# Performance work log

Measured on AMD Instinct MI355X. Metric: run time of the kernel, lower is better.

## Reference

```python
import jax, jax.numpy as jnp
import numpy as np

IMG_SIZE = 640


def _decode_level(cls, box, img_size):
    """cls: [B,C,H,W] logits, box: [B,4,H,W] offsets -> ([B,HW,4], [B,HW,1], [B,HW])."""
    B = cls.shape[0]
    cls = jnp.transpose(cls, (0, 2, 3, 1))          # [B,H,W,C]
    box = jnp.transpose(box, (0, 2, 3, 1))          # [B,H,W,4]
    prob = jax.nn.sigmoid(cls)
    conf = jnp.max(prob, axis=-1, keepdims=True)    # [B,H,W,1]
    cidx = jnp.argmax(prob, axis=-1)                # [B,H,W]
    stage = box.shape[1]                            # H (== W)
    step = img_size // stage                        # stride for this level
    grid = jnp.arange(stage, dtype=box.dtype) * step
    gx, gy = jnp.meshgrid(grid, grid, indexing='xy')
    block = jnp.stack([gx, gy], axis=-1)            # [H,W,2] anchor-point coords
    tl = block - box[..., :2]                       # x1,y1
    br = block + box[..., 2:4]                      # x2,y2
    boxes = jnp.concatenate([tl, br], axis=-1).reshape(B, -1, 4)
    scores = conf.reshape(B, -1, 1)
    classes = cidx.reshape(B, -1).astype(jnp.int64)
    return boxes, scores, classes


def setup_inputs() -> dict:
    key = jax.random.key(0)
    ks = jax.random.split(key, 6)
    return {
        'cls0': jax.random.normal(ks[0], (64, 80, 80, 80), dtype=jnp.float32),
        'box0': jax.random.uniform(ks[1], (64, 4, 80, 80), dtype=jnp.float32) * 32.0,
        'cls1': jax.random.normal(ks[2], (64, 80, 40, 40), dtype=jnp.float32),
        'box1': jax.random.uniform(ks[3], (64, 4, 40, 40), dtype=jnp.float32) * 64.0,
        'cls2': jax.random.normal(ks[4], (64, 80, 20, 20), dtype=jnp.float32),
        'box2': jax.random.uniform(ks[5], (64, 4, 20, 20), dtype=jnp.float32) * 128.0,
    }


def reference(cls0, box0, cls1, box1, cls2, box2):
    levels = [(cls0, box0), (cls1, box1), (cls2, box2)]
    boxes_l, scores_l, classes_l = [], [], []
    for cls, box in levels:
        b, s, c = _decode_level(cls, box, IMG_SIZE)
        boxes_l.append(b)
        scores_l.append(s)
        classes_l.append(c)
    boxes = jnp.concatenate(boxes_l, axis=1)      # [B,N,4]
    scores = jnp.concatenate(scores_l, axis=1)    # [B,N,1]
    classes = jnp.concatenate(classes_l, axis=1)  # [B,N]
    boxes = jnp.clip(boxes, 0.0, IMG_SIZE - 1)
    return boxes, scores, classes
```

## Files before the change

kernel.cpp:

```cpp
#include <hip/hip_runtime.h>
#include <cmath>


constexpr int B_   = 64;
constexpr int NC   = 80;
constexpr int NTOT = 8400;

__device__ __forceinline__ float sigmoidf_(float x) { return 1.0f / (1.0f + __expf(-x)); }

template<int HW, int W, int STEP, int NOFF>
__device__ __forceinline__ void decode_level(
    const float* __restrict__ cls, const float* __restrict__ box,
    float* __restrict__ oboxes, float* __restrict__ oscores, float* __restrict__ oclasses,
    int lbid, int tid)
{
    constexpr int PPI = HW / 2;

    int t = lbid * 256 + tid;
    int b = t / PPI;
    int p = (t - b * PPI) << 1;
    int h = p / W;
    int w = p - h * W;

    const float* bbase = box + (size_t)b * 4 * HW + p;
    float2 bl = *reinterpret_cast<const float2*>(bbase);
    float2 bt = *reinterpret_cast<const float2*>(bbase + HW);
    float2 br = *reinterpret_cast<const float2*>(bbase + 2 * HW);
    float2 bd = *reinterpret_cast<const float2*>(bbase + 3 * HW);

    const float* cbase = cls + (size_t)b * NC * HW + p;
    float m[2]  = {-3.4e38f, -3.4e38f};
    int   ci[2] = {0, 0};
    #pragma unroll 16
    for (int c = 0; c < NC; ++c) {
        float2 v = *reinterpret_cast<const float2*>(cbase + (size_t)c * HW);
        if (v.x > m[0]) { m[0] = v.x; ci[0] = c; }
        if (v.y > m[1]) { m[1] = v.y; ci[1] = c; }
    }

    size_t obase = (size_t)b * NTOT + NOFF + p;
    *reinterpret_cast<float2*>(oscores  + obase) = make_float2(sigmoidf_(m[0]), sigmoidf_(m[1]));
    *reinterpret_cast<float2*>(oclasses + obase) = make_float2((float)ci[0], (float)ci[1]);

    float gy = (float)(h * STEP);
    #pragma unroll
    for (int j = 0; j < 2; ++j) {
        float gx = (float)((w + j) * STEP);
        float l  = j ? bl.y : bl.x;
        float tt = j ? bt.y : bt.x;
        float r  = j ? br.y : br.x;
        float dd = j ? bd.y : bd.x;
        float4 o;
        o.x = fminf(fmaxf(gx - l,  0.0f), 639.0f);
        o.y = fminf(fmaxf(gy - tt, 0.0f), 639.0f);
        o.z = fminf(fmaxf(gx + r,  0.0f), 639.0f);
        o.w = fminf(fmaxf(gy + dd, 0.0f), 639.0f);
        *reinterpret_cast<float4*>(oboxes + (obase + j) * 4) = o;
    }
}

__global__ __launch_bounds__(256) void rtmdet_decode_fused(
    const float* __restrict__ cls0, const float* __restrict__ box0,
    const float* __restrict__ cls1, const float* __restrict__ box1,
    const float* __restrict__ cls2, const float* __restrict__ box2,
    float* __restrict__ oboxes, float* __restrict__ oscores, float* __restrict__ oclasses)
{
    int bid = blockIdx.x;
    int tid = threadIdx.x;
    if (bid < 800) {
        decode_level<6400, 80,  8,    0>(cls0, box0, oboxes, oscores, oclasses, bid,        tid);
    } else if (bid < 1000) {
        decode_level<1600, 40, 16, 6400>(cls1, box1, oboxes, oscores, oclasses, bid - 800,  tid);
    } else {
        decode_level< 400, 20, 32, 8000>(cls2, box2, oboxes, oscores, oclasses, bid - 1000, tid);
    }
}

extern "C" void kernel_launch(void* const* d_in, const int* in_sizes, int n_in,
                              void* d_out, int out_size, void* d_ws, size_t ws_size,
                              hipStream_t stream) {
    const float* cls0 = (const float*)d_in[0];
    const float* box0 = (const float*)d_in[1];
    const float* cls1 = (const float*)d_in[2];
    const float* box1 = (const float*)d_in[3];
    const float* cls2 = (const float*)d_in[4];
    const float* box2 = (const float*)d_in[5];

    float* oboxes   = (float*)d_out;
    float* oscores  = oboxes  + (size_t)B_ * NTOT * 4;
    float* oclasses = oscores + (size_t)B_ * NTOT;

    rtmdet_decode_fused<<<1050, 256, 0, stream>>>(cls0, box0, cls1, box1, cls2, box2,
                                                  oboxes, oscores, oclasses);
}
```

Measured before the change: 33.67 us.

## Split class reduction across two half-blocks with float4 loads and LDS merge

Each block now covers 512 positions as 128 quads. The two halves of the block each take 40 of the 80 classes and read them with float4 loads, then merge their max and argmax through shared memory after a barrier. Box decoding keeps its original pairwise mapping. The intent is wider 16-byte loads and a shorter serial per-thread loop, in exchange for a __syncthreads, LDS traffic, and half the threads sitting idle during the final score write. Grid size and total traffic are unchanged.

```diff
diff --git a/kernel.cpp b/kernel.cpp
--- a/kernel.cpp
+++ b/kernel.cpp
@@ -12,50 +12,86 @@
 __device__ __forceinline__ void decode_level(
     const float* __restrict__ cls, const float* __restrict__ box,
     float* __restrict__ oboxes, float* __restrict__ oscores, float* __restrict__ oclasses,
-    int lbid, int tid)
+    int lbid, int tid,
+    float (* __restrict__ sm)[256], int* __restrict__ spk)
 {
+    constexpr int QPI = HW / 4;
     constexpr int PPI = HW / 2;
 
-    int t = lbid * 256 + tid;
-    int b = t / PPI;
-    int p = (t - b * PPI) << 1;
-    int h = p / W;
-    int w = p - h * W;
+    int half = tid >> 7;
+    int lp   = tid & 127;
+    int quad = lbid * 128 + lp;
+    int b    = quad / QPI;
+    int p    = (quad - b * QPI) << 2;
 
-    const float* bbase = box + (size_t)b * 4 * HW + p;
-    float2 bl = *reinterpret_cast<const float2*>(bbase);
-    float2 bt = *reinterpret_cast<const float2*>(bbase + HW);
-    float2 br = *reinterpret_cast<const float2*>(bbase + 2 * HW);
-    float2 bd = *reinterpret_cast<const float2*>(bbase + 3 * HW);
-
-    const float* cbase = cls + (size_t)b * NC * HW + p;
-    float m[2]  = {-3.4e38f, -3.4e38f};
-    int   ci[2] = {0, 0};
-    #pragma unroll 16
-    for (int c = 0; c < NC; ++c) {
-        float2 v = *reinterpret_cast<const float2*>(cbase + (size_t)c * HW);
-        if (v.x > m[0]) { m[0] = v.x; ci[0] = c; }
-        if (v.y > m[1]) { m[1] = v.y; ci[1] = c; }
+    const float* cbase = cls + (size_t)b * NC * HW + (size_t)(half * 40) * HW + p;
+    float m[4]  = {-3.4e38f, -3.4e38f, -3.4e38f, -3.4e38f};
+    int   ci[4] = {0, 0, 0, 0};
+    #pragma unroll 8
+    for (int c = 0; c < 40; ++c) {
+        float4 v = *reinterpret_cast<const float4*>(cbase + (size_t)c * HW);
+        float vv[4] = {v.x, v.y, v.z, v.w};
+        #pragma unroll
+        for (int j = 0; j < 4; ++j) {
+            if (vv[j] > m[j]) { m[j] = vv[j]; ci[j] = c; }
+        }
     }
 
-    size_t obase = (size_t)b * NTOT + NOFF + p;
-    *reinterpret_cast<float2*>(oscores  + obase) = make_float2(sigmoidf_(m[0]), sigmoidf_(m[1]));
-    *reinterpret_cast<float2*>(oclasses + obase) = make_float2((float)ci[0], (float)ci[1]);
+    #pragma unroll
+    for (int j = 0; j < 4; ++j) sm[j][tid] = m[j];
+    spk[tid] = ci[0] | (ci[1] << 8) | (ci[2] << 16) | (ci[3] << 24);
+    __syncthreads();
 
-    float gy = (float)(h * STEP);
-    #pragma unroll
-    for (int j = 0; j < 2; ++j) {
-        float gx = (float)((w + j) * STEP);
-        float l  = j ? bl.y : bl.x;
-        float tt = j ? bt.y : bt.x;
-        float r  = j ? br.y : br.x;
-        float dd = j ? bd.y : bd.x;
-        float4 o;
-        o.x = fminf(fmaxf(gx - l,  0.0f), 639.0f);
-        o.y = fminf(fmaxf(gy - tt, 0.0f), 639.0f);
-        o.z = fminf(fmaxf(gx + r,  0.0f), 639.0f);
-        o.w = fminf(fmaxf(gy + dd, 0.0f), 639.0f);
-        *reinterpret_cast<float4*>(oboxes + (obase + j) * 4) = o;
+    if (tid < 128) {
+        int pr  = tid + 128;
+        int opk = spk[pr];
+        float4 osc, ocl;
+        float* oscp = &osc.x;
+        float* oclp = &ocl.x;
+        #pragma unroll
+        for (int j = 0; j < 4; ++j) {
+            float om = sm[j][pr];
+            int   oc = ((opk >> (8 * j)) & 0xFF) + 40;
+            float mm = m[j];
+            int   cc = ci[j];
+            if (om > mm) { mm = om; cc = oc; }
+            oscp[j] = sigmoidf_(mm);
+            oclp[j] = (float)cc;
+        }
+        size_t obase = (size_t)b * NTOT + NOFF + p;
+        *reinterpret_cast<float4*>(oscores  + obase) = osc;
+        *reinterpret_cast<float4*>(oclasses + obase) = ocl;
+    }
+
+    {
+        int pair = lbid * 256 + tid;
+        int bb   = pair / PPI;
+        int pp   = (pair - bb * PPI) << 1;
+        int hh   = pp / W;
+        int ww   = pp - hh * W;
+
+        const float* bbase = box + (size_t)bb * 4 * HW + pp;
+        float2 bl = *reinterpret_cast<const float2*>(bbase);
+        float2 bt = *reinterpret_cast<const float2*>(bbase + HW);
+        float2 br = *reinterpret_cast<const float2*>(bbase + 2 * HW);
+        float2 bd = *reinterpret_cast<const float2*>(bbase + 3 * HW);
+
+        float gy = (float)(hh * STEP);
+        size_t ob = (size_t)bb * NTOT + NOFF + pp;
+        #pragma unroll
+        for (int j = 0; j < 2; ++j) {
+            float gx = (float)((ww + j) * STEP);
+            float l  = j ? bl.y : bl.x;
+            float tt = j ? bt.y : bt.x;
+            float r  = j ? br.y : br.x;
+            float dd = j ? bd.y : bd.x;
+            float4 o;
+            o.x = fminf(fmaxf(gx - l,  0.0f), 639.0f);
+            o.y = fminf(fmaxf(gy - tt, 0.0f), 639.0f);
+            o.z = fminf(fmaxf(gx + r,  0.0f), 639.0f);
+            o.w = fminf(fmaxf(gy + dd, 0.0f), 639.0f);
+            *reinterpret_cast<float4*>(oboxes + (ob + j) * 4) = o;
+        }
     }
 }
 
@@ -65,14 +101,20 @@
     const float* __restrict__ cls2, const float* __restrict__ box2,
     float* __restrict__ oboxes, float* __restrict__ oscores, float* __restrict__ oclasses)
 {
+    __shared__ float sm[4][256];
+    __shared__ int   spk[256];
+
     int bid = blockIdx.x;
     int tid = threadIdx.x;
     if (bid < 800) {
-        decode_level<6400, 80,  8,    0>(cls0, box0, oboxes, oscores, oclasses, bid,        tid);
+        decode_level<6400, 80,  8,    0>(cls0, box0, oboxes, oscores, oclasses, bid,
+                                         tid, sm, spk);
     } else if (bid < 1000) {
-        decode_level<1600, 40, 16, 6400>(cls1, box1, oboxes, oscores, oclasses, bid - 800,  tid);
+        decode_level<1600, 40, 16, 6400>(cls1, box1, oboxes, oscores, oclasses, bid - 800,
+                                         tid, sm, spk);
     } else {
-        decode_level< 400, 20, 32, 8000>(cls2, box2, oboxes, oscores, oclasses, bid - 1000, tid);
+        decode_level< 400, 20, 32, 8000>(cls2, box2, oboxes, oscores, oclasses, bid - 1000,
+                                         tid, sm, spk);
     }
 }
 
```

New measurement: 33.71 us. Within noise of the previous version (+0.1%).
